# Kernel tuning notes

Hardware: AMD Instinct MI355X
Metric: run time of the kernel (lower is better)

The kernel has to match this reference:

```python
import jax, jax.numpy as jnp
import numpy as np

B, S, D, H = 4, 2048, 1024, 16
DK = D // H


def setup_inputs() -> dict:
    key = jax.random.key(0)
    ks = jax.random.split(key, 10)
    std = 0.02
    inp = {
        "input": jax.random.normal(ks[0], (B, S, D), dtype=jnp.float32),
        "attention_reweight": jax.random.uniform(ks[1], (B, S), dtype=jnp.float32),
        "mask": 1,
        "Wq": jax.random.normal(ks[2], (D, D), dtype=jnp.float32) * std,
        "bq": jnp.zeros((D,), dtype=jnp.float32),
        "Wk": jax.random.normal(ks[3], (D, D), dtype=jnp.float32) * std,
        "bk": jnp.zeros((D,), dtype=jnp.float32),
        "Wv": jax.random.normal(ks[4], (D, D), dtype=jnp.float32) * std,
        "bv": jnp.zeros((D,), dtype=jnp.float32),
        "Wo": jax.random.normal(ks[5], (D, D), dtype=jnp.float32) * std,
        "bo": jnp.zeros((D,), dtype=jnp.float32),
    }
    return inp


def reference(input, attention_reweight, mask, Wq, bq, Wk, bk, Wv, bv, Wo, bo):
    b, s, d = input.shape
    # QKV projections (torch Linear: x @ W.T + b)
    q = (input @ Wq.T + bq).reshape(b, s, H, DK).transpose(0, 2, 1, 3)  # [B,H,S,dk]
    k = (input @ Wk.T + bk).reshape(b, s, H, DK).transpose(0, 2, 1, 3)
    v = (input @ Wv.T + bv).reshape(b, s, H, DK).transpose(0, 2, 1, 3)

    scores = jnp.einsum("bhqd,bhkd->bhqk", q, k)  # [B,H,S,S]
    if mask:
        causal = jnp.triu(jnp.ones((s, s), dtype=scores.dtype), k=1)
        scores = scores - causal * 1e9
    scores = scores / jnp.sqrt(jnp.asarray(DK, dtype=jnp.float32))
    # reweight per key position: [B,S] broadcast over heads and query positions
    scores = scores * attention_reweight[:, None, None, :]

    attn = jax.nn.softmax(scores, axis=-1)
    out = jnp.einsum("bhqk,bhkd->bhqd", attn, v)  # [B,H,S,dk]
    out = out.transpose(0, 2, 1, 3).reshape(b, s, d)
    return out @ Wo.T + bo
```

## Files before the change

### kernel.cpp

```cpp
#include <hip/hip_runtime.h>
#include <math.h>

#define B_  4
#define S_  2048
#define D_  1024
#define H_  16
#define DK_ 64

typedef __bf16 bf16x8 __attribute__((ext_vector_type(8)));
typedef float  f32x4  __attribute__((ext_vector_type(4)));

__device__ __forceinline__ unsigned short f2bf(float f) {
  unsigned int u = __builtin_bit_cast(unsigned int, f);
  u += 0x7fffu + ((u >> 16) & 1u);
  return (unsigned short)(u >> 16);
}

__device__ __forceinline__ unsigned short bfbits(float f) {
  __bf16 h = (__bf16)f;
  return __builtin_bit_cast(unsigned short, h);
}

__device__ __forceinline__ f32x4 mfma16(bf16x8 a, bf16x8 b, f32x4 c) {
  return __builtin_amdgcn_mfma_f32_16x16x32_bf16(a, b, c, 0, 0, 0);
}

__device__ __forceinline__ void gl_lds16(const unsigned short* g, unsigned short* l) {
  __builtin_amdgcn_global_load_lds(
      (const __attribute__((address_space(1))) void*)g,
      (__attribute__((address_space(3))) void*)l, 16, 0, 0);
}

__global__ void SAA_cast_bf16(const float* __restrict__ src,
                              unsigned short* __restrict__ dst, int n4) {
  int i = blockIdx.x * blockDim.x + threadIdx.x;
  int stride = gridDim.x * blockDim.x;
  for (; i < n4; i += stride) {
    float4 v = reinterpret_cast<const float4*>(src)[i];
    ushort4 o;
    o.x = f2bf(v.x); o.y = f2bf(v.y); o.z = f2bf(v.z); o.w = f2bf(v.w);
    reinterpret_cast<ushort4*>(dst)[i] = o;
  }
}

__global__ void SAA_cast4(const float* __restrict__ s0, const float* __restrict__ s1,
                          const float* __restrict__ s2, const float* __restrict__ s3,
                          unsigned short* __restrict__ d0, unsigned short* __restrict__ d1,
                          unsigned short* __restrict__ d2, unsigned short* __restrict__ d3,
                          int n4) {
  const float* src = (blockIdx.y == 0) ? s0 : (blockIdx.y == 1) ? s1
                   : (blockIdx.y == 2) ? s2 : s3;
  unsigned short* dst = (blockIdx.y == 0) ? d0 : (blockIdx.y == 1) ? d1
                      : (blockIdx.y == 2) ? d2 : d3;
  int i = blockIdx.x * blockDim.x + threadIdx.x;
  int stride = gridDim.x * blockDim.x;
  for (; i < n4; i += stride) {
    float4 v = reinterpret_cast<const float4*>(src)[i];
    ushort4 o;
    o.x = f2bf(v.x); o.y = f2bf(v.y); o.z = f2bf(v.z); o.w = f2bf(v.w);
    reinterpret_cast<ushort4*>(dst)[i] = o;
  }
}

__global__ __launch_bounds__(512)
void SAA_gemm_qkv(const unsigned short* __restrict__ Xb,
                  const unsigned short* __restrict__ Wqb,
                  const unsigned short* __restrict__ Wkb,
                  const unsigned short* __restrict__ Wvb,
                  const float* __restrict__ bq,
                  const float* __restrict__ bk,
                  const float* __restrict__ bv,
                  const float* __restrict__ rw,
                  unsigned short* __restrict__ Qo,
                  unsigned short* __restrict__ Ko,
                  unsigned short* __restrict__ Vto)
{
  const int K = D_;
  __shared__ __attribute__((aligned(16))) unsigned short sA[2][128 * 64];
  __shared__ __attribute__((aligned(16))) unsigned short sB[2][3][128 * 64];

  const int t = threadIdx.x;
  const int w = t >> 6, l = t & 63;
  const int wm = w >> 2, wn = w & 3;
  const int lr = l & 15, lg = l >> 4;
  const int r7 = lr & 7;

  const int m0 = blockIdx.y * 128;
  const int n0 = blockIdx.x * 128;

  const unsigned short* gA  = Xb  + (size_t)m0 * K;
  const unsigned short* gB0 = Wqb + (size_t)n0 * K;
  const unsigned short* gB1 = Wkb + (size_t)n0 * K;
  const unsigned short* gB2 = Wvb + (size_t)n0 * K;

  int srow[2], soff[2];
#pragma unroll
  for (int i = 0; i < 2; i++) {
    const int c = i * 512 + t;
    srow[i] = c >> 3;
    soff[i] = ((c & 7) ^ (srow[i] & 7)) * 8;
  }

#define STAGE(s, k0)                                                          \
  do {                                                                        \
    _Pragma("unroll")                                                         \
    for (int i = 0; i < 2; i++) {                                             \
      const size_t go = (size_t)srow[i] * K + (k0) + soff[i];                 \
      const int dl = (i * 512 + t) * 8;                                       \
      gl_lds16(gA  + go, &sA[s][dl]);                                         \
      gl_lds16(gB0 + go, &sB[s][0][dl]);                                      \
      gl_lds16(gB1 + go, &sB[s][1][dl]);                                      \
      gl_lds16(gB2 + go, &sB[s][2][dl]);                                      \
    }                                                                         \
  } while (0)

  STAGE(0, 0);

  f32x4 acc[3][4][2] = {};

#pragma unroll 2
  for (int T = 0; T < 16; ++T) {
    __syncthreads();
    if (T + 1 < 16) STAGE((T + 1) & 1, (T + 1) * 64);

    const unsigned short* At = sA[T & 1];
#pragma unroll
    for (int ks = 0; ks < 2; ++ks) {
      const int swk = (((ks * 4 + lg) ^ r7) << 3);
      bf16x8 afr[4];
#pragma unroll
      for (int mi = 0; mi < 4; ++mi)
        afr[mi] = *reinterpret_cast<const bf16x8*>(
            &At[(wm * 64 + mi * 16 + lr) * 64 + swk]);
#pragma unroll
      for (int mat = 0; mat < 3; ++mat) {
        const unsigned short* Bt = sB[T & 1][mat];
        bf16x8 bfr[2];
#pragma unroll
        for (int n = 0; n < 2; ++n)
          bfr[n] = *reinterpret_cast<const bf16x8*>(
              &Bt[(wn * 32 + n * 16 + lr) * 64 + swk]);
#pragma unroll
        for (int mi = 0; mi < 4; ++mi)
#pragma unroll
          for (int n = 0; n < 2; ++n)
            acc[mat][mi][n] = mfma16(afr[mi], bfr[n], acc[mat][mi][n]);
      }
    }
  }
#undef STAGE

#pragma unroll
  for (int n = 0; n < 2; ++n) {
    const int col = n0 + wn * 32 + n * 16 + lr;
    const int h = col >> 6, dk = col & 63;
    const float bqv = bq[col], bkv = bk[col], bvv = bv[col];
#pragma unroll
    for (int mi = 0; mi < 4; ++mi) {
#pragma unroll
      for (int r = 0; r < 4; ++r) {
        const int row = m0 + wm * 64 + mi * 16 + lg * 4 + r;
        const int b = row >> 11, s = row & 2047;
        Qo[(((size_t)b * H_ + h) * S_ + s) * DK_ + dk] = bfbits(acc[0][mi][n][r] + bqv);
        Ko[(((size_t)b * H_ + h) * S_ + s) * DK_ + dk] =
            bfbits((acc[1][mi][n][r] + bkv) * (0.18033688011112042f * rw[row]));
        Vto[(((size_t)b * H_ + h) * DK_ + dk) * S_ + s] = bfbits(acc[2][mi][n][r] + bvv);
      }
    }
  }
}

__global__ __launch_bounds__(512)
void SAA_attn(const unsigned short* __restrict__ Q,
              const unsigned short* __restrict__ Kb,
              const unsigned short* __restrict__ Vt,
              const int* __restrict__ maskp,
              unsigned short* __restrict__ Cb)
{
  const int pairid = blockIdx.x;
  const int h = blockIdx.y, b = blockIdx.z;
  const int t = threadIdx.x, w = t >> 6, l = t & 63;
  const int lr = l & 15, lg = l >> 4;
  const int mask = maskp[0];

  __shared__ __attribute__((aligned(16))) unsigned short Kt[2][64 * 64];
  __shared__ __attribute__((aligned(16))) unsigned short Vl[2][64 * 64];
  __shared__ __attribute__((aligned(16))) unsigned short Pl[8][16 * 64];

  const size_t bh = (size_t)b * H_ + h;
  const unsigned short* Qbh = Q + bh * S_ * DK_;
  const unsigned short* Kbh = Kb + bh * S_ * DK_;
  const unsigned short* Vbh = Vt + bh * DK_ * S_;
  unsigned short* Pw = &Pl[w][0];

  const int r0 = t >> 3, cc0 = t & 7;
  const int sw0 = (cc0 ^ (r0 & 7)) * 8;

  for (int half = 0; half < 2; ++half) {
    const int qb = half ? (15 - pairid) : pairid;
    const int q0 = qb * 128;
    const int wq = q0 + w * 16;

    bf16x8 qf[2];
#pragma unroll
    for (int ks = 0; ks < 2; ks++)
      qf[ks] = *reinterpret_cast<const bf16x8*>(
          &Qbh[(size_t)(wq + lr) * DK_ + ks * 32 + lg * 8]);

    f32x4 acc[4] = {};
    float lrun[4] = {0.f, 0.f, 0.f, 0.f};

    const int nkt = mask ? (qb * 2 + 2) : (S_ / 64);
    const int wqmax = wq + 15;

    __syncthreads();

    gl_lds16(Kbh + (size_t)r0 * DK_ + sw0, &Kt[0][t * 8]);
    gl_lds16(Vbh + (size_t)r0 * S_ + sw0,  &Vl[0][t * 8]);
    int cur = 0;

    for (int kt = 0; kt < nkt; ++kt) {
      __syncthreads();
      if (kt + 1 < nkt) {
        const int kn = (kt + 1) * 64;
        const int nb = cur ^ 1;
        gl_lds16(Kbh + (size_t)(kn + r0) * DK_ + sw0, &Kt[nb][t * 8]);
        gl_lds16(Vbh + (size_t)r0 * S_ + kn + sw0,    &Vl[nb][t * 8]);
      }

      const int k0 = kt * 64;
      const bool active = (!mask) || (k0 <= wqmax);
      if (active) {
        const unsigned short* Kc = &Kt[cur][0];
        const unsigned short* Vc = &Vl[cur][0];

        f32x4 sc[4] = {};
#pragma unroll
        for (int ks = 0; ks < 2; ++ks) {
          const int swk = (((ks * 4 + lg) ^ (lr & 7)) << 3);
#pragma unroll
          for (int t2 = 0; t2 < 4; ++t2) {
            bf16x8 kf = *reinterpret_cast<const bf16x8*>(&Kc[(t2 * 16 + lr) * 64 + swk]);
            sc[t2] = mfma16(qf[ks], kf, sc[t2]);
          }
        }

        const bool needmask = mask && (k0 + 63 > wq);

#pragma unroll
        for (int r = 0; r < 4; r++) {
          const int row = wq + lg * 4 + r;
          float v0 = sc[0][r], v1 = sc[1][r];
          float v2 = sc[2][r], v3 = sc[3][r];
          if (needmask) {
            if (k0 + lr      > row) v0 = -1e30f;
            if (k0 + 16 + lr > row) v1 = -1e30f;
            if (k0 + 32 + lr > row) v2 = -1e30f;
            if (k0 + 48 + lr > row) v3 = -1e30f;
          }
          const float p0 = __builtin_amdgcn_exp2f(v0);
          const float p1 = __builtin_amdgcn_exp2f(v1);
          const float p2 = __builtin_amdgcn_exp2f(v2);
          const float p3 = __builtin_amdgcn_exp2f(v3);
          lrun[r] += (p0 + p1) + (p2 + p3);
          const int prow = lg * 4 + r;
          const int pr7 = prow & 7;
          const int pbase = prow * 64 + (lr & 7);
          const int hi = lr >> 3;
          Pw[pbase + (((0 + hi) ^ pr7) << 3)] = bfbits(p0);
          Pw[pbase + (((2 + hi) ^ pr7) << 3)] = bfbits(p1);
          Pw[pbase + (((4 + hi) ^ pr7) << 3)] = bfbits(p2);
          Pw[pbase + (((6 + hi) ^ pr7) << 3)] = bfbits(p3);
        }

#pragma unroll
        for (int ks = 0; ks < 2; ++ks) {
          const int swk = (((ks * 4 + lg) ^ (lr & 7)) << 3);
          bf16x8 pf = *reinterpret_cast<const bf16x8*>(&Pw[lr * 64 + swk]);
#pragma unroll
          for (int dt = 0; dt < 4; ++dt) {
            bf16x8 vf = *reinterpret_cast<const bf16x8*>(&Vc[(dt * 16 + lr) * 64 + swk]);
            acc[dt] = mfma16(pf, vf, acc[dt]);
          }
        }
      }
      cur ^= 1;
    }

#pragma unroll
    for (int r = 0; r < 4; r++) {
      float rs = lrun[r];
      rs += __shfl_xor(rs, 1);
      rs += __shfl_xor(rs, 2);
      rs += __shfl_xor(rs, 4);
      rs += __shfl_xor(rs, 8);
      lrun[r] = __builtin_amdgcn_rcpf(rs);
    }
#pragma unroll
    for (int dt = 0; dt < 4; dt++) {
#pragma unroll
      for (int r = 0; r < 4; r++) {
        const int row = wq + lg * 4 + r;
        const int col = h * DK_ + dt * 16 + lr;
        Cb[((size_t)b * S_ + row) * D_ + col] = bfbits(acc[dt][r] * lrun[r]);
      }
    }
  }
}

__global__ __launch_bounds__(256)
void SAA_gemm_out(const unsigned short* __restrict__ Cb,
                  const unsigned short* __restrict__ Wob,
                  const float* __restrict__ bo,
                  float* __restrict__ Y)
{
  const int K = D_;
  __shared__ __attribute__((aligned(16))) unsigned short lA[2][128 * 64];
  __shared__ __attribute__((aligned(16))) unsigned short lB[2][128 * 64];

  const int t = threadIdx.x;
  const int w = t >> 6, l = t & 63;
  const int wr = w >> 1, wc = w & 1;
  const int lr = l & 15, lg = l >> 4;
  const int r7 = lr & 7;

  const int m0 = blockIdx.y * 128;
  const int n0 = blockIdx.x * 128;

  const unsigned short* gA = Cb + (size_t)m0 * K;
  const unsigned short* gB = Wob + (size_t)n0 * K;

  int srow[4], soff[4];
#pragma unroll
  for (int i = 0; i < 4; i++) {
    const int c = i * 256 + t;
    srow[i] = c >> 3;
    soff[i] = ((c & 7) ^ (srow[i] & 7)) * 8;
  }

#define STAGEO(s, k0)                                                         \
  do {                                                                        \
    _Pragma("unroll")                                                         \
    for (int i = 0; i < 4; i++) {                                             \
      const size_t go = (size_t)srow[i] * K + (k0) + soff[i];                 \
      const int dl = (i * 256 + t) * 8;                                       \
      gl_lds16(gA + go, &lA[s][dl]);                                          \
      gl_lds16(gB + go, &lB[s][dl]);                                          \
    }                                                                         \
  } while (0)

  STAGEO(0, 0);

  f32x4 acc[4][4] = {};

#pragma unroll 2
  for (int T = 0; T < 16; ++T) {
    __syncthreads();
    if (T + 1 < 16) STAGEO((T + 1) & 1, (T + 1) * 64);

    const unsigned short* At = lA[T & 1];
    const unsigned short* Bt = lB[T & 1];
#pragma unroll
    for (int ks = 0; ks < 2; ks++) {
      const int swk = (((ks * 4 + lg) ^ r7) << 3);
      bf16x8 af[4], bfr[4];
#pragma unroll
      for (int i = 0; i < 4; i++)
        af[i] = *reinterpret_cast<const bf16x8*>(&At[(wr * 64 + i * 16 + lr) * 64 + swk]);
#pragma unroll
      for (int j = 0; j < 4; j++)
        bfr[j] = *reinterpret_cast<const bf16x8*>(&Bt[(wc * 64 + j * 16 + lr) * 64 + swk]);
#pragma unroll
      for (int i = 0; i < 4; i++)
#pragma unroll
        for (int j = 0; j < 4; j++)
          acc[i][j] = mfma16(af[i], bfr[j], acc[i][j]);
    }
  }
#undef STAGEO

#pragma unroll
  for (int j = 0; j < 4; j++) {
    const int col = n0 + wc * 64 + j * 16 + lr;
    const float bsv = bo[col];
#pragma unroll
    for (int i = 0; i < 4; i++) {
#pragma unroll
      for (int r = 0; r < 4; r++) {
        const int row = m0 + wr * 64 + i * 16 + lg * 4 + r;
        Y[(size_t)row * D_ + col] = acc[i][j][r] + bsv;
      }
    }
  }
}

extern "C" void kernel_launch(void* const* d_in, const int* in_sizes, int n_in,
                              void* d_out, int out_size, void* d_ws, size_t ws_size,
                              hipStream_t stream) {
  const float* input = (const float*)d_in[0];
  const float* rw    = (const float*)d_in[1];
  const int*   maskp = (const int*)d_in[2];
  const float* Wq = (const float*)d_in[3];
  const float* bq = (const float*)d_in[4];
  const float* Wk = (const float*)d_in[5];
  const float* bk = (const float*)d_in[6];
  const float* Wv = (const float*)d_in[7];
  const float* bv = (const float*)d_in[8];
  const float* Wo = (const float*)d_in[9];
  const float* bo = (const float*)d_in[10];

  char* ws = (char*)d_ws;
  unsigned short* Xb  = (unsigned short*)(ws);
  unsigned short* Wqb = (unsigned short*)(ws + (16u << 20));
  unsigned short* Wkb = (unsigned short*)(ws + (18u << 20));
  unsigned short* Wvb = (unsigned short*)(ws + (20u << 20));
  unsigned short* Wob = (unsigned short*)(ws + (22u << 20));
  unsigned short* Qo  = (unsigned short*)(ws + (24u << 20));
  unsigned short* Ko  = (unsigned short*)(ws + (40u << 20));
  unsigned short* Vto = (unsigned short*)(ws + (56u << 20));
  unsigned short* Cb  = Xb;

  SAA_cast_bf16<<<2048, 256, 0, stream>>>(input, Xb, (B_ * S_ * D_) / 4);
  SAA_cast4<<<dim3(512, 4), 256, 0, stream>>>(Wq, Wk, Wv, Wo, Wqb, Wkb, Wvb, Wob,
                                              (D_ * D_) / 4);

  SAA_gemm_qkv<<<dim3(8, 64), 512, 0, stream>>>(Xb, Wqb, Wkb, Wvb, bq, bk, bv, rw,
                                                Qo, Ko, Vto);
  SAA_attn<<<dim3(8, 16, 4), 512, 0, stream>>>(Qo, Ko, Vto, maskp, Cb);
  SAA_gemm_out<<<dim3(8, 64), 256, 0, stream>>>(Cb, Wob, bo, (float*)d_out);
}
```

Measured before the change: 184.4 us.

## Merge cast kernels and retile output GEMM to 512x64 blocks

Combines the input and weight bf16 cast kernels into one launch with a 5-way grid, removing one kernel launch. The output projection GEMM moves from 128x128 tiles with 256 threads to 512x64 tiles with 512 threads, where each wave owns 64 rows and all waves share one 64-column B tile. This changes A/B reuse and grid shape (256 blocks instead of 512). The trade-off is larger LDS use (about 144KB double-buffered), which limits occupancy, and the input cast now runs on only 512 blocks, which may be slower.

```diff
diff --git a/kernel.cpp b/kernel.cpp
--- a/kernel.cpp
+++ b/kernel.cpp
@@ -31,27 +31,17 @@
       (__attribute__((address_space(3))) void*)l, 16, 0, 0);
 }
 
-__global__ void SAA_cast_bf16(const float* __restrict__ src,
-                              unsigned short* __restrict__ dst, int n4) {
-  int i = blockIdx.x * blockDim.x + threadIdx.x;
-  int stride = gridDim.x * blockDim.x;
-  for (; i < n4; i += stride) {
-    float4 v = reinterpret_cast<const float4*>(src)[i];
-    ushort4 o;
-    o.x = f2bf(v.x); o.y = f2bf(v.y); o.z = f2bf(v.z); o.w = f2bf(v.w);
-    reinterpret_cast<ushort4*>(dst)[i] = o;
-  }
-}
-
-__global__ void SAA_cast4(const float* __restrict__ s0, const float* __restrict__ s1,
-                          const float* __restrict__ s2, const float* __restrict__ s3,
-                          unsigned short* __restrict__ d0, unsigned short* __restrict__ d1,
-                          unsigned short* __restrict__ d2, unsigned short* __restrict__ d3,
-                          int n4) {
-  const float* src = (blockIdx.y == 0) ? s0 : (blockIdx.y == 1) ? s1
-                   : (blockIdx.y == 2) ? s2 : s3;
-  unsigned short* dst = (blockIdx.y == 0) ? d0 : (blockIdx.y == 1) ? d1
-                      : (blockIdx.y == 2) ? d2 : d3;
+__global__ void SAA_cast_all(const float* __restrict__ x,
+                             const float* __restrict__ s1, const float* __restrict__ s2,
+                             const float* __restrict__ s3, const float* __restrict__ s4,
+                             unsigned short* __restrict__ dx,
+                             unsigned short* __restrict__ d1, unsigned short* __restrict__ d2,
+                             unsigned short* __restrict__ d3, unsigned short* __restrict__ d4)
+{
+  const int y = blockIdx.y;
+  const float* src = (y == 0) ? x : (y == 1) ? s1 : (y == 2) ? s2 : (y == 3) ? s3 : s4;
+  unsigned short* dst = (y == 0) ? dx : (y == 1) ? d1 : (y == 2) ? d2 : (y == 3) ? d3 : d4;
+  const int n4 = (y == 0) ? (B_ * S_ * D_) / 4 : (D_ * D_) / 4;
   int i = blockIdx.x * blockDim.x + threadIdx.x;
   int stride = gridDim.x * blockDim.x;
   for (; i < n4; i += stride) {
@@ -308,45 +298,37 @@
   }
 }
 
-__global__ __launch_bounds__(256)
+__global__ __launch_bounds__(512)
 void SAA_gemm_out(const unsigned short* __restrict__ Cb,
                   const unsigned short* __restrict__ Wob,
                   const float* __restrict__ bo,
                   float* __restrict__ Y)
 {
   const int K = D_;
-  __shared__ __attribute__((aligned(16))) unsigned short lA[2][128 * 64];
-  __shared__ __attribute__((aligned(16))) unsigned short lB[2][128 * 64];
+  __shared__ __attribute__((aligned(16))) unsigned short lA[2][512 * 64];
+  __shared__ __attribute__((aligned(16))) unsigned short lB[2][64 * 64];
 
   const int t = threadIdx.x;
   const int w = t >> 6, l = t & 63;
-  const int wr = w >> 1, wc = w & 1;
   const int lr = l & 15, lg = l >> 4;
   const int r7 = lr & 7;
 
-  const int m0 = blockIdx.y * 128;
-  const int n0 = blockIdx.x * 128;
+  const int m0 = blockIdx.y * 512;
+  const int n0 = blockIdx.x * 64;
 
   const unsigned short* gA = Cb + (size_t)m0 * K;
   const unsigned short* gB = Wob + (size_t)n0 * K;
 
-  int srow[4], soff[4];
-#pragma unroll
-  for (int i = 0; i < 4; i++) {
-    const int c = i * 256 + t;
-    srow[i] = c >> 3;
-    soff[i] = ((c & 7) ^ (srow[i] & 7)) * 8;
-  }
+  const int sr = t >> 3;
+  const int soff = ((t & 7) ^ (sr & 7)) * 8;
 
 #define STAGEO(s, k0)                                                         \
   do {                                                                        \
     _Pragma("unroll")                                                         \
-    for (int i = 0; i < 4; i++) {                                             \
-      const size_t go = (size_t)srow[i] * K + (k0) + soff[i];                 \
-      const int dl = (i * 256 + t) * 8;                                       \
-      gl_lds16(gA + go, &lA[s][dl]);                                          \
-      gl_lds16(gB + go, &lB[s][dl]);                                          \
-    }                                                                         \
+    for (int i = 0; i < 8; i++)                                               \
+      gl_lds16(gA + (size_t)(i * 64 + sr) * K + (k0) + soff,                  \
+               &lA[s][(i * 512 + t) * 8]);                                    \
+    gl_lds16(gB + (size_t)sr * K + (k0) + soff, &lB[s][t * 8]);               \
   } while (0)
 
   STAGEO(0, 0);
@@ -366,10 +348,10 @@
       bf16x8 af[4], bfr[4];
 #pragma unroll
       for (int i = 0; i < 4; i++)
-        af[i] = *reinterpret_cast<const bf16x8*>(&At[(wr * 64 + i * 16 + lr) * 64 + swk]);
+        af[i] = *reinterpret_cast<const bf16x8*>(&At[(w * 64 + i * 16 + lr) * 64 + swk]);
 #pragma unroll
       for (int j = 0; j < 4; j++)
-        bfr[j] = *reinterpret_cast<const bf16x8*>(&Bt[(wc * 64 + j * 16 + lr) * 64 + swk]);
+        bfr[j] = *reinterpret_cast<const bf16x8*>(&Bt[(j * 16 + lr) * 64 + swk]);
 #pragma unroll
       for (int i = 0; i < 4; i++)
 #pragma unroll
@@ -381,13 +363,13 @@
 
 #pragma unroll
   for (int j = 0; j < 4; j++) {
-    const int col = n0 + wc * 64 + j * 16 + lr;
+    const int col = n0 + j * 16 + lr;
     const float bsv = bo[col];
 #pragma unroll
     for (int i = 0; i < 4; i++) {
 #pragma unroll
       for (int r = 0; r < 4; r++) {
-        const int row = m0 + wr * 64 + i * 16 + lg * 4 + r;
+        const int row = m0 + w * 64 + i * 16 + lg * 4 + r;
         Y[(size_t)row * D_ + col] = acc[i][j][r] + bsv;
       }
     }
@@ -420,12 +402,11 @@
   unsigned short* Vto = (unsigned short*)(ws + (56u << 20));
   unsigned short* Cb  = Xb;
 
-  SAA_cast_bf16<<<2048, 256, 0, stream>>>(input, Xb, (B_ * S_ * D_) / 4);
-  SAA_cast4<<<dim3(512, 4), 256, 0, stream>>>(Wq, Wk, Wv, Wo, Wqb, Wkb, Wvb, Wob,
-                                              (D_ * D_) / 4);
+  SAA_cast_all<<<dim3(512, 5), 256, 0, stream>>>(input, Wq, Wk, Wv, Wo,
+                                                 Xb, Wqb, Wkb, Wvb, Wob);
 
   SAA_gemm_qkv<<<dim3(8, 64), 512, 0, stream>>>(Xb, Wqb, Wkb, Wvb, bq, bk, bv, rw,
                                                 Qo, Ko, Vto);
   SAA_attn<<<dim3(8, 16, 4), 512, 0, stream>>>(Qo, Ko, Vto, maskp, Cb);
-  SAA_gemm_out<<<dim3(8, 64), 256, 0, stream>>>(Cb, Wob, bo, (float*)d_out);
-}
+  SAA_gemm_out<<<dim3(16, 16), 512, 0, stream>>>(Cb, Wob, bo, (float*)d_out);
+}
```

Measured after the change: 184.6 us. Within noise of the previous version (+0.1%).
